# Performance work log

Hardware: AMD Instinct MI355X
Metric: run time of the kernel (lower is better)

The kernel has to match this reference:

```python
import jax, jax.numpy as jnp
import numpy as np

B, N, D = 8, 512, 1024
E, H, TOP_K = 8, 8, 2
HD = D // H
EPS = 1e-5


def setup_inputs() -> dict:
    key = jax.random.key(0)
    ks = jax.random.split(key, 8)
    # kaiming_uniform with a=sqrt(5) over fan_in=N -> bound = sqrt(6/((1+5)*N)) = 1/sqrt(N)
    bound_w = 1.0 / np.sqrt(N)
    bound_lin = 1.0 / np.sqrt(D)
    return {
        "x": jax.random.normal(ks[0], (B, N, D), dtype=jnp.float32),
        "weight": jax.random.uniform(ks[1], (E, H, N, N), jnp.float32, -bound_w, bound_w),
        "bias": jnp.zeros((E, H, N), jnp.float32),
        "router_w": jax.random.uniform(ks[2], (E, D), jnp.float32, -bound_lin, bound_lin),
        "in_w": jax.random.uniform(ks[3], (D, D), jnp.float32, -bound_lin, bound_lin),
        "in_b": jax.random.uniform(ks[4], (D,), jnp.float32, -bound_lin, bound_lin),
        "out_w": jax.random.uniform(ks[5], (D, D), jnp.float32, -bound_lin, bound_lin),
        "out_b": jax.random.uniform(ks[6], (D,), jnp.float32, -bound_lin, bound_lin),
    }


def reference(x, weight, bias, router_w, in_w, in_b, out_w, out_b):
    # Router: mean-pool tokens, linear, softmax, top-k
    router_logits = x.mean(axis=1) @ router_w.T              # (B, E)
    router_probs = jax.nn.softmax(router_logits, axis=-1)
    top_w, top_i = jax.lax.top_k(router_probs, TOP_K)        # (B, K)
    top_w = top_w / top_w.sum(axis=-1, keepdims=True)

    # Input projection -> (B, H, hd, N), layer-norm over token axis N (no affine)
    xp = x @ in_w.T + in_b                                   # (B, N, D)
    xr = xp.reshape(B, N, H, HD).transpose(0, 2, 3, 1)       # (B, H, hd, N)
    mu = xr.mean(axis=-1, keepdims=True)
    var = xr.var(axis=-1, keepdims=True)
    xn = (xr - mu) * jax.lax.rsqrt(var + EPS)

    # Gather per-(batch, head, k) NxN expert matrices, row-softmax
    w = weight[top_i].transpose(0, 2, 1, 3, 4)               # (B, H, K, N, N)
    b = bias[top_i].transpose(0, 2, 1, 3)                    # (B, H, K, N)
    w_attn = jax.nn.softmax(w, axis=-1)

    # out[b,h,k,d,m] = sum_n xn[b,h,d,n] * w_attn[b,h,k,m,n]
    out = jnp.einsum('bhdn,bhkmn->bhkdm', xn, w_attn)
    out = out + b[:, :, :, None, :]                          # (B, H, K, hd, N)
    out = (out * top_w[:, None, :, None, None]).sum(axis=2)  # (B, H, hd, N)

    out = out.transpose(0, 3, 1, 2).reshape(B, N, D)         # (B, N, D)
    out = out @ out_w.T + out_b

    # Load-balancing aux loss
    top1 = top_i[:, 0]
    expert_mask = jax.nn.one_hot(top1, E, dtype=jnp.float32)
    aux = E * (router_probs.mean(axis=0) * expert_mask.mean(axis=0)).sum()
    return out, aux
```

## Files before the change

### kernel.cpp

```cpp
#include <hip/hip_runtime.h>
#include <hip/hip_bf16.h>

#define Bv 8
#define Nv 512
#define Dv 1024
#define Ev 8
#define Hv 8
#define HDv 128
#define EPSv 1e-5f

typedef __attribute__((ext_vector_type(8))) short short8;
typedef __attribute__((ext_vector_type(4))) float f32x4;

__device__ __forceinline__ unsigned short f2b(float f) {
    __hip_bfloat16 h = __float2bfloat16(f);
    return *reinterpret_cast<unsigned short*>(&h);
}
__device__ __forceinline__ float bf2f(unsigned int u) {
    union { unsigned int i; float f; } v; v.i = u << 16; return v.f;
}
__device__ __forceinline__ unsigned int blend2(unsigned int a, unsigned int b,
                                               float tw0, float tw1) {
    float lo = tw0 * bf2f(a & 0xffffu) + tw1 * bf2f(b & 0xffffu);
    float hi = tw0 * bf2f(a >> 16)     + tw1 * bf2f(b >> 16);
    return (unsigned int)f2b(lo) | ((unsigned int)f2b(hi) << 16);
}

__device__ __forceinline__ void gld16(const void* g, void* l) {
    __builtin_amdgcn_global_load_lds(
        (const __attribute__((address_space(1))) void*)(uintptr_t)(g),
        (__attribute__((address_space(3))) void*)(uintptr_t)(l), 16, 0, 0);
}

__global__ __launch_bounds__(256) void k_preA(const float* __restrict__ x,
                                              const float* __restrict__ w1,
                                              unsigned short* __restrict__ xb,
                                              float* __restrict__ part_x,
                                              unsigned short* __restrict__ w1b) {
    int bid = blockIdx.x;
    int t = threadIdx.x;
    if (bid < 128) {
        int b = bid >> 4, c = bid & 15;
        const float* px = x + ((size_t)b * Nv + c * 32) * Dv + t * 4;
        unsigned short* qx = xb + ((size_t)b * Nv + c * 32) * Dv + t * 4;
        float4 s4 = make_float4(0.f, 0.f, 0.f, 0.f);
        #pragma unroll 8
        for (int r = 0; r < 32; ++r) {
            float4 v = *(const float4*)(px + (size_t)r * Dv);
            s4.x += v.x; s4.y += v.y; s4.z += v.z; s4.w += v.w;
            uint2 pk;
            pk.x = (unsigned)f2b(v.x) | ((unsigned)f2b(v.y) << 16);
            pk.y = (unsigned)f2b(v.z) | ((unsigned)f2b(v.w) << 16);
            *(uint2*)(qx + (size_t)r * Dv) = pk;
        }
        *(float4*)(part_x + ((size_t)(b * 16 + c)) * Dv + t * 4) = s4;
        return;
    }
    int base = (bid - 128) * 8192;
    #pragma unroll
    for (int i = 0; i < 8; ++i) {
        float4 a = *(const float4*)(w1 + base + i * 1024 + t * 4);
        uint2 p;
        p.x = (unsigned)f2b(a.x) | ((unsigned)f2b(a.y) << 16);
        p.y = (unsigned)f2b(a.z) | ((unsigned)f2b(a.w) << 16);
        *(uint2*)(w1b + base + i * 1024 + t * 4) = p;
    }
}

__global__ __launch_bounds__(256) void k_g1s(
    const unsigned short* __restrict__ A,
    const unsigned short* __restrict__ W,
    const float* __restrict__ bias,
    unsigned short* __restrict__ Cv,
    float2* __restrict__ part,
    const float* __restrict__ part_x,
    float* __restrict__ xmean,
    const float* __restrict__ weight,
    unsigned short* __restrict__ wa,
    const float* __restrict__ w2,
    unsigned short* __restrict__ w2b) {
    __shared__ __align__(16) unsigned short sh[2][2][128 * 64];
    const int bid = blockIdx.x;
    const int t = threadIdx.x;

    if (bid >= 256) {
        if (bid < 1280) {
            int lane = t & 63;
            int r0 = (((bid - 256) * 4) + (t >> 6)) * 8;
            const float* wp = weight + (size_t)r0 * Nv + lane * 4;
            float v[8][8];
            #pragma unroll
            for (int r = 0; r < 8; ++r) {
                float4 a = *(const float4*)(wp + (size_t)r * Nv);
                float4 b = *(const float4*)(wp + (size_t)r * Nv + 256);
                v[r][0] = a.x; v[r][1] = a.y; v[r][2] = a.z; v[r][3] = a.w;
                v[r][4] = b.x; v[r][5] = b.y; v[r][6] = b.z; v[r][7] = b.w;
            }
            float sm[8];
            #pragma unroll
            for (int r = 0; r < 8; ++r) {
                #pragma unroll
                for (int i = 0; i < 8; ++i) v[r][i] = __expf(v[r][i]);
                float s01 = v[r][0] + v[r][1], s23 = v[r][2] + v[r][3];
                float s45 = v[r][4] + v[r][5], s67 = v[r][6] + v[r][7];
                sm[r] = (s01 + s23) + (s45 + s67);
            }
            for (int off = 1; off < 64; off <<= 1) {
                #pragma unroll
                for (int r = 0; r < 8; ++r) sm[r] += __shfl_xor(sm[r], off);
            }
            unsigned short* wq = wa + (size_t)r0 * Nv + lane * 4;
            #pragma unroll
            for (int r = 0; r < 8; ++r) {
                float inv = 1.f / sm[r];
                uint2 p0, p1;
                p0.x = (unsigned)f2b(v[r][0] * inv) | ((unsigned)f2b(v[r][1] * inv) << 16);
                p0.y = (unsigned)f2b(v[r][2] * inv) | ((unsigned)f2b(v[r][3] * inv) << 16);
                p1.x = (unsigned)f2b(v[r][4] * inv) | ((unsigned)f2b(v[r][5] * inv) << 16);
                p1.y = (unsigned)f2b(v[r][6] * inv) | ((unsigned)f2b(v[r][7] * inv) << 16);
                *(uint2*)(wq + (size_t)r * Nv) = p0;
                *(uint2*)(wq + (size_t)r * Nv + 256) = p1;
            }
            return;
        }
        int base = (bid - 1280) * 8192;
        #pragma unroll
        for (int i = 0; i < 8; ++i) {
            float4 a = *(const float4*)(w2 + base + i * 1024 + t * 4);
            uint2 p;
            p.x = (unsigned)f2b(a.x) | ((unsigned)f2b(a.y) << 16);
            p.y = (unsigned)f2b(a.z) | ((unsigned)f2b(a.w) << 16);
            *(uint2*)(w2b + base + i * 1024 + t * 4) = p;
        }
        return;
    }

    const int bn = (bid & 7) * 128;
    const int bm = (bid >> 3) * 128;
    const int lane = t & 63;
    const int w = t >> 6, wm = w >> 1, wn = w & 1;
    const int fr = lane & 15, fq = lane >> 4;
    const int K = Dv, NT = 16;
    f32x4 acc[4][4] = {};

#define STAGE2(s, k0)                                                       \
    {                                                                       \
        _Pragma("unroll")                                                   \
        for (int i_ = 0; i_ < 4; ++i_) {                                    \
            int c_ = t + i_ * 256;                                          \
            int row_ = c_ >> 3, col_ = c_ & 7;                              \
            int cs_ = col_ ^ (row_ & 7);                                    \
            gld16(A + (size_t)(bm + row_) * K + (k0) + cs_ * 8, &sh[0][s][c_ * 8]); \
            gld16(W + (size_t)(bn + row_) * K + (k0) + cs_ * 8, &sh[1][s][c_ * 8]); \
        }                                                                   \
    }

    STAGE2(0, 0);
    {
        int o = bid * 32 + (t >> 3);
        int c2 = t & 7;
        int b2 = o >> 10, d2 = o & 1023;
        float S = part_x[((size_t)(b2 * 16 + c2)) * Dv + d2]
                + part_x[((size_t)(b2 * 16 + c2 + 8)) * Dv + d2];
        S += __shfl_xor(S, 1); S += __shfl_xor(S, 2); S += __shfl_xor(S, 4);
        if (c2 == 0) xmean[o] = S * (1.f / Nv);
    }
    for (int it = 0; it < NT; ++it) {
        if (it + 1 < NT) {
            STAGE2((it + 1) & 1, (it + 1) * 64);
            asm volatile("s_waitcnt vmcnt(8)" ::: "memory");
        } else {
            asm volatile("s_waitcnt vmcnt(0)" ::: "memory");
        }
        __builtin_amdgcn_s_barrier();
        const unsigned short* pA = sh[0][it & 1];
        const unsigned short* pB = sh[1][it & 1];
        #pragma unroll
        for (int kk = 0; kk < 2; ++kk) {
            short8 af[4], bv[4];
            #pragma unroll
            for (int i = 0; i < 4; ++i)
                af[i] = *(const short8*)&pA[(wm * 64 + i * 16 + fr) * 64 + (((kk << 2) + fq) ^ (fr & 7)) * 8];
            #pragma unroll
            for (int j = 0; j < 4; ++j)
                bv[j] = *(const short8*)&pB[(wn * 64 + j * 16 + fr) * 64 + (((kk << 2) + fq) ^ (fr & 7)) * 8];
            #pragma unroll
            for (int i = 0; i < 4; ++i)
                #pragma unroll
                for (int j = 0; j < 4; ++j)
                    acc[i][j] = __builtin_amdgcn_mfma_f32_16x16x32_bf16(af[i], bv[j], acc[i][j], 0, 0, 0);
        }
        __builtin_amdgcn_s_barrier();
    }
#undef STAGE2

    unsigned short* sc = &sh[0][0][0];
    float2* red = (float2*)((char*)&sh[0][0][0] + 36864);
    const int bB   = bm >> 9;
    const int tok0 = bm & 511;
    const int chunk = (bm >> 7) & 3;
    #pragma unroll
    for (int j = 0; j < 4; ++j) {
        const int col = wn * 64 + j * 16 + fr;
        const float bj = bias[bn + col];
        float s = 0.f, q = 0.f;
        #pragma unroll
        for (int i = 0; i < 4; ++i) {
            const int row0 = wm * 64 + i * 16 + fq * 4;
            #pragma unroll
            for (int r = 0; r < 4; r += 2) {
                float v0 = acc[i][j][r] + bj;
                float v1 = acc[i][j][r + 1] + bj;
                s += v0 + v1;
                q = fmaf(v0, v0, fmaf(v1, v1, q));
                unsigned int pk = (unsigned int)f2b(v0) | ((unsigned int)f2b(v1) << 16);
                *(unsigned int*)&sc[col * 136 + row0 + r] = pk;
            }
        }
        red[col * 8 + wm * 4 + fq] = make_float2(s, q);
    }
    __syncthreads();
    if (t < 128) {
        float S = 0.f, Q = 0.f;
        #pragma unroll
        for (int k = 0; k < 8; ++k) { float2 v = red[t * 8 + k]; S += v.x; Q += v.y; }
        part[((size_t)bB * Dv + bn + t) * 4 + chunk] = make_float2(S, Q);
    }
    #pragma unroll
    for (int k = 0; k < 8; ++k) {
        const int c = t + k * 256;
        const int dl = c >> 4, tk = c & 15;
        uint4 v = *(const uint4*)&sc[dl * 136 + tk * 8];
        *(uint4*)&Cv[((size_t)bB * Dv + bn + dl) * Nv + tok0 + tk * 8] = v;
    }
}

__global__ __launch_bounds__(256) void k_mixg(
    const unsigned short* __restrict__ wa,
    const unsigned short* __restrict__ xpT,
    const float* __restrict__ bias,
    const float* __restrict__ xmean,
    const float* __restrict__ router_w,
    const float2* __restrict__ part,
    unsigned short* __restrict__ y,
    float* __restrict__ aux_out) {
    __shared__ __align__(16) unsigned short sA[2][128 * 64];
    __shared__ __align__(16) unsigned short sB[2][128 * 64];
    __shared__ float probs[Bv][Ev];
    __shared__ float twsh[Bv][2];
    __shared__ int   tsel[Bv][2];
    __shared__ int   top1s[Bv];
    const int t = threadIdx.x;
    const int bm = blockIdx.x * 128;
    const int bh = blockIdx.y;
    const int b = bh >> 3, h = bh & 7;

    {
        int pid = t >> 2, l = t & 3;
        int rb = pid >> 3, re = pid & 7;
        const float4* xm = (const float4*)(xmean + rb * Dv);
        const float4* rw = (const float4*)(router_w + re * Dv);
        float s = 0.f;
        #pragma unroll
        for (int j = 0; j < 64; ++j) {
            float4 aa = xm[l + j * 4], ww = rw[l + j * 4];
            s = fmaf(aa.x, ww.x, s); s = fmaf(aa.y, ww.y, s);
            s = fmaf(aa.z, ww.z, s); s = fmaf(aa.w, ww.w, s);
        }
        s += __shfl_xor(s, 1); s += __shfl_xor(s, 2);
        if (l == 0) probs[rb][re] = s;
    }
    __syncthreads();
    if (t < Bv) {
        int bb = t;
        float mx = -1e30f;
        for (int e2 = 0; e2 < Ev; ++e2) mx = fmaxf(mx, probs[bb][e2]);
        float sum = 0.f;
        for (int e2 = 0; e2 < Ev; ++e2) { float v = __expf(probs[bb][e2] - mx); probs[bb][e2] = v; sum += v; }
        float inv = 1.f / sum;
        for (int e2 = 0; e2 < Ev; ++e2) probs[bb][e2] *= inv;
        int i0 = 0; float p0 = probs[bb][0];
        for (int e2 = 1; e2 < Ev; ++e2) if (probs[bb][e2] > p0) { p0 = probs[bb][e2]; i0 = e2; }
        int i1 = -1; float p1 = -1.f;
        for (int e2 = 0; e2 < Ev; ++e2) if (e2 != i0 && probs[bb][e2] > p1) { p1 = probs[bb][e2]; i1 = e2; }
        float s2 = p0 + p1;
        tsel[bb][0] = i0; tsel[bb][1] = i1;
        twsh[bb][0] = p0 / s2; twsh[bb][1] = p1 / s2;
        top1s[bb] = i0;
    }
    __syncthreads();
    if (blockIdx.x == 0 && bh == 0 && t == 0) {
        float aux = 0.f;
        for (int e2 = 0; e2 < Ev; ++e2) {
            float pm = 0.f, mm = 0.f;
            for (int bb = 0; bb < Bv; ++bb) { pm += probs[bb][e2]; mm += (top1s[bb] == e2) ? 1.f : 0.f; }
            aux += (pm / Bv) * (mm / Bv);
        }
        *aux_out = aux * Ev;
    }
    const int e0 = tsel[b][0], e1 = tsel[b][1];
    const float tw0 = twsh[b][0], tw1 = twsh[b][1];

    const int lane = t & 63;
    const int w = t >> 6, wm = w >> 1, wn = w & 1;
    const int fr = lane & 15, fq = lane >> 4;

    float rstd_j[4], nmr_j[4];
    #pragma unroll
    for (int j = 0; j < 4; ++j) {
        const int dg = h * HDv + wn * 64 + j * 16 + fr;
        const float2* pp = part + ((size_t)b * Dv + dg) * 4;
        float S = 0.f, Q = 0.f;
        #pragma unroll
        for (int cc = 0; cc < 4; ++cc) { float2 v = pp[cc]; S += v.x; Q += v.y; }
        float mu = S * (1.f / Nv);
        float var = Q * (1.f / Nv) - mu * mu;
        float rs = rsqrtf(var + EPSv);
        rstd_j[j] = rs; nmr_j[j] = -mu * rs;
    }

    const unsigned short* A0 = wa + (size_t)(e0 * Hv + h) * Nv * Nv;
    const unsigned short* A1 = wa + (size_t)(e1 * Hv + h) * Nv * Nv;
    const unsigned short* Bb = xpT + ((size_t)b * Dv + h * HDv) * Nv;
    const int NT = Nv >> 6;
    f32x4 acc[4][4] = {};
    uint4 ra0[4], ra1[4];

#define BSTAGE(s, k0)                                                       \
    {                                                                       \
        _Pragma("unroll")                                                   \
        for (int i_ = 0; i_ < 4; ++i_) {                                    \
            int c_ = t + i_ * 256;                                          \
            int row_ = c_ >> 3, col_ = c_ & 7;                              \
            int cs_ = col_ ^ (row_ & 7);                                    \
            gld16(Bb + (size_t)row_ * Nv + (k0) + cs_ * 8, &sB[s][c_ * 8]); \
        }                                                                   \
    }
#define ALOAD(k0)                                                           \
    {                                                                       \
        _Pragma("unroll")                                                   \
        for (int i_ = 0; i_ < 4; ++i_) {                                    \
            int c_ = t + i_ * 256;                                          \
            int row_ = c_ >> 3, col_ = c_ & 7;                              \
            int cs_ = col_ ^ (row_ & 7);                                    \
            size_t off_ = (size_t)(bm + row_) * Nv + (k0) + cs_ * 8;        \
            ra0[i_] = *(const uint4*)&A0[off_];                             \
            ra1[i_] = *(const uint4*)&A1[off_];                             \
        }                                                                   \
    }

    BSTAGE(0, 0);
    ALOAD(0);
    for (int it = 0; it < NT; ++it) {
        if (it + 1 < NT) {
            BSTAGE((it + 1) & 1, (it + 1) * 64);
            asm volatile("s_waitcnt vmcnt(4)" ::: "memory");
        } else {
            asm volatile("s_waitcnt vmcnt(0)" ::: "memory");
        }
        #pragma unroll
        for (int i = 0; i < 4; ++i) {
            int c = t + i * 256;
            uint4 o;
            o.x = blend2(ra0[i].x, ra1[i].x, tw0, tw1);
            o.y = blend2(ra0[i].y, ra1[i].y, tw0, tw1);
            o.z = blend2(ra0[i].z, ra1[i].z, tw0, tw1);
            o.w = blend2(ra0[i].w, ra1[i].w, tw0, tw1);
            *(uint4*)&sA[it & 1][c * 8] = o;
        }
        if (it + 1 < NT) ALOAD((it + 1) * 64);
        asm volatile("s_waitcnt lgkmcnt(0)" ::: "memory");
        __builtin_amdgcn_s_barrier();
        const unsigned short* pA = sA[it & 1];
        const unsigned short* pB = sB[it & 1];
        #pragma unroll
        for (int kk = 0; kk < 2; ++kk) {
            short8 af[4], bv[4];
            #pragma unroll
            for (int i = 0; i < 4; ++i)
                af[i] = *(const short8*)&pA[(wm * 64 + i * 16 + fr) * 64 + (((kk << 2) + fq) ^ (fr & 7)) * 8];
            #pragma unroll
            for (int j = 0; j < 4; ++j)
                bv[j] = *(const short8*)&pB[(wn * 64 + j * 16 + fr) * 64 + (((kk << 2) + fq) ^ (fr & 7)) * 8];
            #pragma unroll
            for (int i = 0; i < 4; ++i)
                #pragma unroll
                for (int j = 0; j < 4; ++j)
                    acc[i][j] = __builtin_amdgcn_mfma_f32_16x16x32_bf16(af[i], bv[j], acc[i][j], 0, 0, 0);
        }
        __builtin_amdgcn_s_barrier();
    }
#undef BSTAGE
#undef ALOAD
    #pragma unroll
    for (int i = 0; i < 4; ++i) {
        #pragma unroll
        for (int r = 0; r < 4; ++r) {
            const int m = bm + wm * 64 + i * 16 + fq * 4 + r;
            const float br = tw0 * bias[(size_t)(e0 * Hv + h) * Nv + m]
                           + tw1 * bias[(size_t)(e1 * Hv + h) * Nv + m];
            #pragma unroll
            for (int j = 0; j < 4; ++j) {
                const int d = wn * 64 + j * 16 + fr;
                float v = fmaf(acc[i][j][r], rstd_j[j], nmr_j[j] + br);
                y[((size_t)b * Nv + m) * Dv + h * HDv + d] = f2b(v);
            }
        }
    }
}

__global__ __launch_bounds__(256) void k_gemm0(
    const unsigned short* __restrict__ A,
    const unsigned short* __restrict__ W,
    const float* __restrict__ bias,
    float* __restrict__ C) {
    __shared__ __align__(16) unsigned short sA[3][128 * 64];
    __shared__ __align__(16) unsigned short sB[3][128 * 64];
    const int t = threadIdx.x;
    const int bn = blockIdx.x * 128;
    const int bm = blockIdx.y * 128;
    const int lane = t & 63;
    const int w = t >> 6, wm = w >> 1, wn = w & 1;
    const int fr = lane & 15, fq = lane >> 4;
    const int K = Dv, NT = 16, Nn = Dv;
    f32x4 acc[4][4] = {};

#define STAGE(s, k0)                                                        \
    {                                                                       \
        _Pragma("unroll")                                                   \
        for (int i_ = 0; i_ < 4; ++i_) {                                    \
            int c_ = t + i_ * 256;                                          \
            int row_ = c_ >> 3, col_ = c_ & 7;                              \
            int cs_ = col_ ^ (row_ & 7);                                    \
            gld16(A + (size_t)(bm + row_) * K + (k0) + cs_ * 8, &sA[s][c_ * 8]); \
            gld16(W + (size_t)(bn + row_) * K + (k0) + cs_ * 8, &sB[s][c_ * 8]); \
        }                                                                   \
    }

    STAGE(0, 0);
    STAGE(1, 64);
    for (int it = 0; it < NT; ++it) {
        if (it + 2 < NT) {
            STAGE((it + 2) % 3, (it + 2) * 64);
            asm volatile("s_waitcnt vmcnt(16)" ::: "memory");
        } else if (it + 1 < NT) {
            asm volatile("s_waitcnt vmcnt(8)" ::: "memory");
        } else {
            asm volatile("s_waitcnt vmcnt(0)" ::: "memory");
        }
        __builtin_amdgcn_s_barrier();
        const unsigned short* pA = sA[it % 3];
        const unsigned short* pB = sB[it % 3];
        #pragma unroll
        for (int kk = 0; kk < 2; ++kk) {
            short8 af[4], bv[4];
            #pragma unroll
            for (int i = 0; i < 4; ++i)
                af[i] = *(const short8*)&pA[(wm * 64 + i * 16 + fr) * 64 + (((kk << 2) + fq) ^ (fr & 7)) * 8];
            #pragma unroll
            for (int j = 0; j < 4; ++j)
                bv[j] = *(const short8*)&pB[(wn * 64 + j * 16 + fr) * 64 + (((kk << 2) + fq) ^ (fr & 7)) * 8];
            #pragma unroll
            for (int i = 0; i < 4; ++i)
                #pragma unroll
                for (int j = 0; j < 4; ++j)
                    acc[i][j] = __builtin_amdgcn_mfma_f32_16x16x32_bf16(af[i], bv[j], acc[i][j], 0, 0, 0);
        }
        __builtin_amdgcn_s_barrier();
    }
#undef STAGE
    #pragma unroll
    for (int j = 0; j < 4; ++j) {
        const int n = bn + wn * 64 + j * 16 + fr;
        const float bj = bias[n];
        #pragma unroll
        for (int i = 0; i < 4; ++i) {
            const int m0 = bm + wm * 64 + i * 16 + fq * 4;
            #pragma unroll
            for (int r = 0; r < 4; ++r)
                C[(size_t)(m0 + r) * Nn + n] = acc[i][j][r] + bj;
        }
    }
}

extern "C" void kernel_launch(void* const* d_in, const int* in_sizes, int n_in,
                              void* d_out, int out_size, void* d_ws, size_t ws_size,
                              hipStream_t stream) {
    const float* x        = (const float*)d_in[0];
    const float* weight   = (const float*)d_in[1];
    const float* bias     = (const float*)d_in[2];
    const float* router_w = (const float*)d_in[3];
    const float* in_w     = (const float*)d_in[4];
    const float* in_b     = (const float*)d_in[5];
    const float* out_w    = (const float*)d_in[6];
    const float* out_b    = (const float*)d_in[7];
    float* out = (float*)d_out;

    if (ws_size < ((size_t)63 << 20)) return;

    char* wsb = (char*)d_ws;
    float*  xmean  = (float*)(wsb);
    float2* part   = (float2*)(wsb + (64 << 10));
    float*  part_x = (float*)(wsb + (512 << 10));
    unsigned short* in_wb  = (unsigned short*)(wsb + ((size_t)2 << 20));
    unsigned short* out_wb = (unsigned short*)(wsb + ((size_t)4 << 20));
    unsigned short* xb     = (unsigned short*)(wsb + ((size_t)8 << 20));
    unsigned short* xpT    = (unsigned short*)(wsb + ((size_t)16 << 20));
    unsigned short* wa     = (unsigned short*)(wsb + ((size_t)24 << 20));
    unsigned short* y = xb;

    k_preA<<<256, 256, 0, stream>>>(x, in_w, xb, part_x, in_wb);
    k_g1s<<<1408, 256, 0, stream>>>(xb, in_wb, in_b, xpT, part, part_x, xmean,
                                    weight, wa, out_w, out_wb);
    k_mixg<<<dim3(4, 64), 256, 0, stream>>>(wa, xpT, bias, xmean, router_w, part, y,
                                            out + (size_t)Bv * Nv * Dv);
    k_gemm0<<<dim3(8, 32), 256, 0, stream>>>(y, out_wb, out_b, out);
}
```

Baseline: 77.03 us.

## Fuse fp32-to-bf16 conversion into input GEMM and compute token mean via atomics

Removes the separate pre-conversion kernel. The input-projection GEMM now loads fp32 x and in_w directly, converts them to bf16 in registers and stores them to a single LDS buffer, instead of using async global-to-LDS copies of pre-converted bf16 data. The token-sum for the router is computed by extra blocks with atomicAdd into a memset buffer, and the 1/N scaling moves into the router kernel. This saves a launch and a bf16 round trip through memory, but it drops LDS double-buffering, doubles global read bytes per tile because the loads are fp32, and re-reads in_w in fp32 for every tile.

```diff
diff --git a/kernel.cpp b/kernel.cpp
--- a/kernel.cpp
+++ b/kernel.cpp
@@ -32,61 +32,40 @@
         (__attribute__((address_space(3))) void*)(uintptr_t)(l), 16, 0, 0);
 }
 
-__global__ __launch_bounds__(256) void k_preA(const float* __restrict__ x,
-                                              const float* __restrict__ w1,
-                                              unsigned short* __restrict__ xb,
-                                              float* __restrict__ part_x,
-                                              unsigned short* __restrict__ w1b) {
-    int bid = blockIdx.x;
-    int t = threadIdx.x;
-    if (bid < 128) {
-        int b = bid >> 4, c = bid & 15;
-        const float* px = x + ((size_t)b * Nv + c * 32) * Dv + t * 4;
-        unsigned short* qx = xb + ((size_t)b * Nv + c * 32) * Dv + t * 4;
-        float4 s4 = make_float4(0.f, 0.f, 0.f, 0.f);
-        #pragma unroll 8
-        for (int r = 0; r < 32; ++r) {
-            float4 v = *(const float4*)(px + (size_t)r * Dv);
-            s4.x += v.x; s4.y += v.y; s4.z += v.z; s4.w += v.w;
-            uint2 pk;
-            pk.x = (unsigned)f2b(v.x) | ((unsigned)f2b(v.y) << 16);
-            pk.y = (unsigned)f2b(v.z) | ((unsigned)f2b(v.w) << 16);
-            *(uint2*)(qx + (size_t)r * Dv) = pk;
-        }
-        *(float4*)(part_x + ((size_t)(b * 16 + c)) * Dv + t * 4) = s4;
-        return;
-    }
-    int base = (bid - 128) * 8192;
-    #pragma unroll
-    for (int i = 0; i < 8; ++i) {
-        float4 a = *(const float4*)(w1 + base + i * 1024 + t * 4);
-        uint2 p;
-        p.x = (unsigned)f2b(a.x) | ((unsigned)f2b(a.y) << 16);
-        p.y = (unsigned)f2b(a.z) | ((unsigned)f2b(a.w) << 16);
-        *(uint2*)(w1b + base + i * 1024 + t * 4) = p;
-    }
-}
-
-__global__ __launch_bounds__(256) void k_g1s(
-    const unsigned short* __restrict__ A,
-    const unsigned short* __restrict__ W,
-    const float* __restrict__ bias,
-    unsigned short* __restrict__ Cv,
+__global__ __launch_bounds__(256) void k_fused1(
+    const float* __restrict__ x,
+    const float* __restrict__ w1,
+    const float* __restrict__ weight,
+    const float* __restrict__ w2,
+    const float* __restrict__ in_b,
+    unsigned short* __restrict__ xpT,
     float2* __restrict__ part,
-    const float* __restrict__ part_x,
     float* __restrict__ xmean,
-    const float* __restrict__ weight,
     unsigned short* __restrict__ wa,
-    const float* __restrict__ w2,
     unsigned short* __restrict__ w2b) {
-    __shared__ __align__(16) unsigned short sh[2][2][128 * 64];
+    __shared__ __align__(16) unsigned short sh[21504];
     const int bid = blockIdx.x;
     const int t = threadIdx.x;
 
     if (bid >= 256) {
-        if (bid < 1280) {
+        if (bid < 384) {
+            int xb2 = bid - 256;
+            int b = xb2 >> 4, c = xb2 & 15;
+            const float* px = x + ((size_t)b * Nv + c * 32) * Dv + t * 4;
+            float4 s4 = make_float4(0.f, 0.f, 0.f, 0.f);
+            #pragma unroll 8
+            for (int r = 0; r < 32; ++r) {
+                float4 v = *(const float4*)(px + (size_t)r * Dv);
+                s4.x += v.x; s4.y += v.y; s4.z += v.z; s4.w += v.w;
+            }
+            float* xm = xmean + b * Dv + t * 4;
+            atomicAdd(xm + 0, s4.x); atomicAdd(xm + 1, s4.y);
+            atomicAdd(xm + 2, s4.z); atomicAdd(xm + 3, s4.w);
+            return;
+        }
+        if (bid < 1408) {
             int lane = t & 63;
-            int r0 = (((bid - 256) * 4) + (t >> 6)) * 8;
+            int r0 = (((bid - 384) * 4) + (t >> 6)) * 8;
             const float* wp = weight + (size_t)r0 * Nv + lane * 4;
             float v[8][8];
             #pragma unroll
@@ -123,7 +102,7 @@
             }
             return;
         }
-        int base = (bid - 1280) * 8192;
+        int base = (bid - 1408) * 8192;
         #pragma unroll
         for (int i = 0; i < 8; ++i) {
             float4 a = *(const float4*)(w2 + base + i * 1024 + t * 4);
@@ -135,55 +114,65 @@
         return;
     }
 
+    unsigned short* sAs = sh;
+    unsigned short* sBs = sh + 8192;
     const int bn = (bid & 7) * 128;
     const int bm = (bid >> 3) * 128;
     const int lane = t & 63;
     const int w = t >> 6, wm = w >> 1, wn = w & 1;
     const int fr = lane & 15, fq = lane >> 4;
-    const int K = Dv, NT = 16;
     f32x4 acc[4][4] = {};
-
-#define STAGE2(s, k0)                                                       \
+    float4 rx[4][2], rw4[4][2];
+
+#define GLOADF(k0)                                                          \
     {                                                                       \
         _Pragma("unroll")                                                   \
         for (int i_ = 0; i_ < 4; ++i_) {                                    \
             int c_ = t + i_ * 256;                                          \
             int row_ = c_ >> 3, col_ = c_ & 7;                              \
             int cs_ = col_ ^ (row_ & 7);                                    \
-            gld16(A + (size_t)(bm + row_) * K + (k0) + cs_ * 8, &sh[0][s][c_ * 8]); \
-            gld16(W + (size_t)(bn + row_) * K + (k0) + cs_ * 8, &sh[1][s][c_ * 8]); \
+            const float* pa_ = x + (size_t)(bm + row_) * Dv + (k0) + cs_ * 8;  \
+            rx[i_][0] = *(const float4*)pa_;                                \
+            rx[i_][1] = *(const float4*)(pa_ + 4);                          \
+            const float* pw_ = w1 + (size_t)(bn + row_) * Dv + (k0) + cs_ * 8; \
+            rw4[i_][0] = *(const float4*)pw_;                               \
+            rw4[i_][1] = *(const float4*)(pw_ + 4);                         \
         }                                                                   \
     }
-
-    STAGE2(0, 0);
-    {
-        int o = bid * 32 + (t >> 3);
-        int c2 = t & 7;
-        int b2 = o >> 10, d2 = o & 1023;
-        float S = part_x[((size_t)(b2 * 16 + c2)) * Dv + d2]
-                + part_x[((size_t)(b2 * 16 + c2 + 8)) * Dv + d2];
-        S += __shfl_xor(S, 1); S += __shfl_xor(S, 2); S += __shfl_xor(S, 4);
-        if (c2 == 0) xmean[o] = S * (1.f / Nv);
-    }
-    for (int it = 0; it < NT; ++it) {
-        if (it + 1 < NT) {
-            STAGE2((it + 1) & 1, (it + 1) * 64);
-            asm volatile("s_waitcnt vmcnt(8)" ::: "memory");
-        } else {
-            asm volatile("s_waitcnt vmcnt(0)" ::: "memory");
-        }
+#define PACKST()                                                            \
+    {                                                                       \
+        _Pragma("unroll")                                                   \
+        for (int i_ = 0; i_ < 4; ++i_) {                                    \
+            int c_ = t + i_ * 256;                                          \
+            uint4 pa_, pw_;                                                 \
+            pa_.x = (unsigned)f2b(rx[i_][0].x) | ((unsigned)f2b(rx[i_][0].y) << 16); \
+            pa_.y = (unsigned)f2b(rx[i_][0].z) | ((unsigned)f2b(rx[i_][0].w) << 16); \
+            pa_.z = (unsigned)f2b(rx[i_][1].x) | ((unsigned)f2b(rx[i_][1].y) << 16); \
+            pa_.w = (unsigned)f2b(rx[i_][1].z) | ((unsigned)f2b(rx[i_][1].w) << 16); \
+            pw_.x = (unsigned)f2b(rw4[i_][0].x) | ((unsigned)f2b(rw4[i_][0].y) << 16); \
+            pw_.y = (unsigned)f2b(rw4[i_][0].z) | ((unsigned)f2b(rw4[i_][0].w) << 16); \
+            pw_.z = (unsigned)f2b(rw4[i_][1].x) | ((unsigned)f2b(rw4[i_][1].y) << 16); \
+            pw_.w = (unsigned)f2b(rw4[i_][1].z) | ((unsigned)f2b(rw4[i_][1].w) << 16); \
+            *(uint4*)&sAs[c_ * 8] = pa_;                                    \
+            *(uint4*)&sBs[c_ * 8] = pw_;                                    \
+        }                                                                   \
+    }
+
+    GLOADF(0);
+    for (int it = 0; it < 16; ++it) {
+        PACKST();
+        if (it + 1 < 16) GLOADF((it + 1) * 64);
+        asm volatile("s_waitcnt lgkmcnt(0)" ::: "memory");
         __builtin_amdgcn_s_barrier();
-        const unsigned short* pA = sh[0][it & 1];
-        const unsigned short* pB = sh[1][it & 1];
         #pragma unroll
         for (int kk = 0; kk < 2; ++kk) {
             short8 af[4], bv[4];
             #pragma unroll
             for (int i = 0; i < 4; ++i)
-                af[i] = *(const short8*)&pA[(wm * 64 + i * 16 + fr) * 64 + (((kk << 2) + fq) ^ (fr & 7)) * 8];
+                af[i] = *(const short8*)&sAs[(wm * 64 + i * 16 + fr) * 64 + (((kk << 2) + fq) ^ (fr & 7)) * 8];
             #pragma unroll
             for (int j = 0; j < 4; ++j)
-                bv[j] = *(const short8*)&pB[(wn * 64 + j * 16 + fr) * 64 + (((kk << 2) + fq) ^ (fr & 7)) * 8];
+                bv[j] = *(const short8*)&sBs[(wn * 64 + j * 16 + fr) * 64 + (((kk << 2) + fq) ^ (fr & 7)) * 8];
             #pragma unroll
             for (int i = 0; i < 4; ++i)
                 #pragma unroll
@@ -192,17 +181,18 @@
         }
         __builtin_amdgcn_s_barrier();
     }
-#undef STAGE2
-
-    unsigned short* sc = &sh[0][0][0];
-    float2* red = (float2*)((char*)&sh[0][0][0] + 36864);
+#undef GLOADF
+#undef PACKST
+
+    unsigned short* sc = sh;
+    float2* red = (float2*)(sh + 17408);
     const int bB   = bm >> 9;
     const int tok0 = bm & 511;
     const int chunk = (bm >> 7) & 3;
     #pragma unroll
     for (int j = 0; j < 4; ++j) {
         const int col = wn * 64 + j * 16 + fr;
-        const float bj = bias[bn + col];
+        const float bj = in_b[bn + col];
         float s = 0.f, q = 0.f;
         #pragma unroll
         for (int i = 0; i < 4; ++i) {
@@ -231,7 +221,7 @@
         const int c = t + k * 256;
         const int dl = c >> 4, tk = c & 15;
         uint4 v = *(const uint4*)&sc[dl * 136 + tk * 8];
-        *(uint4*)&Cv[((size_t)bB * Dv + bn + dl) * Nv + tok0 + tk * 8] = v;
+        *(uint4*)&xpT[((size_t)bB * Dv + bn + dl) * Nv + tok0 + tk * 8] = v;
     }
 }
 
@@ -268,7 +258,7 @@
             s = fmaf(aa.z, ww.z, s); s = fmaf(aa.w, ww.w, s);
         }
         s += __shfl_xor(s, 1); s += __shfl_xor(s, 2);
-        if (l == 0) probs[rb][re] = s;
+        if (l == 0) probs[rb][re] = s * (1.f / Nv);
     }
     __syncthreads();
     if (t < Bv) {
@@ -501,17 +491,14 @@
     char* wsb = (char*)d_ws;
     float*  xmean  = (float*)(wsb);
     float2* part   = (float2*)(wsb + (64 << 10));
-    float*  part_x = (float*)(wsb + (512 << 10));
-    unsigned short* in_wb  = (unsigned short*)(wsb + ((size_t)2 << 20));
     unsigned short* out_wb = (unsigned short*)(wsb + ((size_t)4 << 20));
-    unsigned short* xb     = (unsigned short*)(wsb + ((size_t)8 << 20));
+    unsigned short* y      = (unsigned short*)(wsb + ((size_t)8 << 20));
     unsigned short* xpT    = (unsigned short*)(wsb + ((size_t)16 << 20));
     unsigned short* wa     = (unsigned short*)(wsb + ((size_t)24 << 20));
-    unsigned short* y = xb;
-
-    k_preA<<<256, 256, 0, stream>>>(x, in_w, xb, part_x, in_wb);
-    k_g1s<<<1408, 256, 0, stream>>>(xb, in_wb, in_b, xpT, part, part_x, xmean,
-                                    weight, wa, out_w, out_wb);
+
+    hipMemsetAsync(xmean, 0, (size_t)Bv * Dv * sizeof(float), stream);
+    k_fused1<<<1536, 256, 0, stream>>>(x, in_w, weight, out_w, in_b,
+                                       xpT, part, xmean, wa, out_wb);
     k_mixg<<<dim3(4, 64), 256, 0, stream>>>(wa, xpT, bias, xmean, router_w, part, y,
                                             out + (size_t)Bv * Nv * Dv);
     k_gemm0<<<dim3(8, 32), 256, 0, stream>>>(y, out_wb, out_b, out);
```

Measured after the change: 83.35 us. +8.2%, slower.
